# Performance work log

Measured on AMD Instinct MI355X. Metric: run time of the kernel, lower is better.

Reference implementation:

```python
import jax, jax.numpy as jnp
import numpy as np

DMODEL, DK, HEADS, FF = 512, 64, 8, 2048
HD = HEADS * DK  # 512; heads are NOT split in this module
EPS = 1e-5


def layernorm(x, g, b):
    mu = jnp.mean(x, axis=-1, keepdims=True)
    var = jnp.mean(jnp.square(x - mu), axis=-1, keepdims=True)
    return (x - mu) * jax.lax.rsqrt(var + EPS) * g + b


def setup_inputs() -> dict:
    key = jax.random.key(0)
    ks = jax.random.split(key, 20)
    s = 1.0 / np.sqrt(DMODEL)
    u = lambda k, shape, fan: jax.random.uniform(k, shape, jnp.float32, -1.0 / np.sqrt(fan), 1.0 / np.sqrt(fan))
    return {
        "x": jax.random.normal(ks[0], (4, 4096, DMODEL), jnp.float32),
        "Wq_w": u(ks[1], (DMODEL, HD), DMODEL), "Wq_b": u(ks[2], (HD,), DMODEL),
        "Wk_w": u(ks[3], (DMODEL, HD), DMODEL), "Wk_b": u(ks[4], (HD,), DMODEL),
        "Wv_w": u(ks[5], (DMODEL, HD), DMODEL), "Wv_b": u(ks[6], (HD,), DMODEL),
        "Wu_w": u(ks[7], (HD, DMODEL), HD), "Wu_b": u(ks[8], (DMODEL,), HD),
        "ln1_g": jnp.ones((DMODEL,), jnp.float32), "ln1_b": jnp.zeros((DMODEL,), jnp.float32),
        "ff1_w": u(ks[9], (DMODEL, FF), DMODEL), "ff1_b": u(ks[10], (FF,), DMODEL),
        "ff2_w": u(ks[11], (FF, DMODEL), FF), "ff2_b": u(ks[12], (DMODEL,), FF),
        "ln2_g": jnp.ones((DMODEL,), jnp.float32), "ln2_b": jnp.zeros((DMODEL,), jnp.float32),
    }


def reference(x, Wq_w, Wq_b, Wk_w, Wk_b, Wv_w, Wv_b, Wu_w, Wu_b,
              ln1_g, ln1_b, ff1_w, ff1_b, ff2_w, ff2_b, ln2_g, ln2_b):
    # x: (b, n, dmodel). Single encoder layer, faithful to num_encoders=1.
    q = x @ Wq_w + Wq_b            # (b, n, HD)
    k = x @ Wk_w + Wk_b
    v = x @ Wv_w + Wv_b
    # NOTE: original does bmm over full HD dim (no head split), scaled by sqrt(dk)
    scores = jnp.einsum('bnd,bmd->bnm', q, k) / np.sqrt(DK)
    probs = jax.nn.softmax(scores, axis=-1)   # (b, n, n) — O(n^2) materialized as in source
    attn = jnp.einsum('bnm,bmd->bnd', probs, v)
    unified = attn @ Wu_w + Wu_b
    h = layernorm(x + unified, ln1_g, ln1_b)
    ffwd = jax.nn.relu(h @ ff1_w + ff1_b) @ ff2_w + ff2_b
    return layernorm(h + ffwd, ln2_g, ln2_b)
```

## Files before the change

kernel.cpp:

```cpp
#include <hip/hip_runtime.h>

#define AS1 __attribute__((address_space(1)))
#define AS3 __attribute__((address_space(3)))

typedef __attribute__((ext_vector_type(8))) short short8;
typedef __attribute__((ext_vector_type(4))) float floatx4;

__device__ __forceinline__ float b2f(ushort u) {
  union { unsigned int i; float f; } x; x.i = ((unsigned int)u) << 16; return x.f;
}
__device__ __forceinline__ ushort f2b(float f) {
  union { float f; unsigned int i; } x; x.f = f;
  unsigned int r = (x.i + 0x7fffu + ((x.i >> 16) & 1u)) >> 16;
  return (ushort)r;
}

#define GF_RELU 1


__global__ __launch_bounds__(256) void gemm_vw(
    const ushort* __restrict__ qkv, const ushort* __restrict__ wut,
    ushort* __restrict__ vwt)
{
  __shared__ __align__(16) ushort As[128 * 32];
  __shared__ __align__(16) ushort Bs[128 * 32];

  const int id = blockIdx.x;
  const int b  = id >> 7;
  const int t  = id & 127;
  const int bx = t & 31;
  const int by = t >> 5;

  const ushort* A  = wut;
  const ushort* Bt = qkv + (size_t)b * 4096 * 1536 + 1024;
  ushort* C = vwt + (size_t)b * 512 * 4096;

  const int tid  = threadIdx.x;
  const int w    = tid >> 6;
  const int lane = tid & 63;
  const int lo   = lane & 15;
  const int quad = lane >> 4;
  const int m0   = by * 128;
  const int n0   = bx * 128;
  const int wm   = (w & 1) * 64;
  const int wn   = (w >> 1) * 64;

  const int i0 = tid, i1 = tid + 256;
  const ushort* ga0 = A  + (size_t)(m0 + (i0 >> 2)) * 512 + ((i0 & 3) << 3);
  const ushort* ga1 = A  + (size_t)(m0 + (i1 >> 2)) * 512 + ((i1 & 3) << 3);
  const ushort* gb0 = Bt + (size_t)(n0 + (i0 >> 2)) * 1536 + ((i0 & 3) << 3);
  const ushort* gb1 = Bt + (size_t)(n0 + (i1 >> 2)) * 1536 + ((i1 & 3) << 3);

  floatx4 acc[4][4] = {};

  for (int k0 = 0; k0 < 512; k0 += 32) {
    __syncthreads();
    __builtin_amdgcn_global_load_lds((const AS1 void*)(ga0 + k0), (AS3 void*)(As + i0 * 8), 16, 0, 0);
    __builtin_amdgcn_global_load_lds((const AS1 void*)(ga1 + k0), (AS3 void*)(As + i1 * 8), 16, 0, 0);
    __builtin_amdgcn_global_load_lds((const AS1 void*)(gb0 + k0), (AS3 void*)(Bs + i0 * 8), 16, 0, 0);
    __builtin_amdgcn_global_load_lds((const AS1 void*)(gb1 + k0), (AS3 void*)(Bs + i1 * 8), 16, 0, 0);
    __syncthreads();

    short8 af[4], bf[4];
#pragma unroll
    for (int tt = 0; tt < 4; ++tt) {
      af[tt] = *(const short8*)(As + (wm + tt * 16 + lo) * 32 + quad * 8);
      bf[tt] = *(const short8*)(Bs + (wn + tt * 16 + lo) * 32 + quad * 8);
    }
#pragma unroll
    for (int mt = 0; mt < 4; ++mt)
#pragma unroll
      for (int nt = 0; nt < 4; ++nt)
        acc[mt][nt] = __builtin_amdgcn_mfma_f32_16x16x32_bf16(af[mt], bf[nt], acc[mt][nt], 0, 0, 0);
  }

#pragma unroll
  for (int mt = 0; mt < 4; ++mt)
#pragma unroll
    for (int nt = 0; nt < 4; ++nt)
#pragma unroll
      for (int r = 0; r < 4; ++r) {
        const int row = m0 + wm + mt * 16 + quad * 4 + r;
        const int col = n0 + wn + nt * 16 + lo;
        C[(size_t)row * 4096 + col] = f2b(acc[mt][nt][r]);
      }
}

__global__ __launch_bounds__(256) void gemm_qk_exp(
    const ushort* __restrict__ qkv, ushort* __restrict__ P)
{
  __shared__ __align__(16) ushort As[128 * 64];
  __shared__ __align__(16) ushort Bs[128 * 64];

  const int id = blockIdx.x;
  const int b  = id >> 10;
  const int t  = id & 1023;
  const int r8 = t & 7;
  const int s2 = t >> 3;
  const int bx = s2 & 31;
  const int by = r8 + ((s2 >> 5) << 3);

  const ushort* A  = qkv + (size_t)b * 4096 * 1536;
  const ushort* Bt = qkv + (size_t)b * 4096 * 1536 + 512;
  ushort* C = P + (size_t)b * 4096 * 4096;

  const int tid  = threadIdx.x;
  const int w    = tid >> 6;
  const int lane = tid & 63;
  const int lo   = lane & 15;
  const int quad = lane >> 4;
  const int m0   = by * 128;
  const int n0   = bx * 128;
  const int wm   = (w & 1) * 64;
  const int wn   = (w >> 1) * 64;

  const ushort* gaP[4]; const ushort* gbP[4];
#pragma unroll
  for (int k = 0; k < 4; ++k) {
    const int s_ = tid + k * 256;
    const int row = s_ >> 3, sl = s_ & 7;
    gaP[k] = A  + (size_t)(m0 + row) * 1536 + ((sl ^ (row & 7)) << 3);
    gbP[k] = Bt + (size_t)(n0 + row) * 1536 + ((sl ^ (row & 7)) << 3);
  }

  floatx4 acc[4][4] = {};

  for (int k0 = 0; k0 < 512; k0 += 64) {
    __syncthreads();
#pragma unroll
    for (int k = 0; k < 4; ++k) {
      const int s_ = tid + k * 256;
      __builtin_amdgcn_global_load_lds((const AS1 void*)(gaP[k] + k0), (AS3 void*)(As + s_ * 8), 16, 0, 0);
      __builtin_amdgcn_global_load_lds((const AS1 void*)(gbP[k] + k0), (AS3 void*)(Bs + s_ * 8), 16, 0, 0);
    }
    __syncthreads();

#pragma unroll
    for (int kk = 0; kk < 2; ++kk) {
      short8 af[4], bf[4];
#pragma unroll
      for (int tt = 0; tt < 4; ++tt) {
        const int ra = wm + tt * 16 + lo;
        const int rb = wn + tt * 16 + lo;
        af[tt] = *(const short8*)(As + (size_t)ra * 64 + (((kk * 4 + quad) ^ (ra & 7)) << 3));
        bf[tt] = *(const short8*)(Bs + (size_t)rb * 64 + (((kk * 4 + quad) ^ (rb & 7)) << 3));
      }
#pragma unroll
      for (int mt = 0; mt < 4; ++mt)
#pragma unroll
        for (int nt = 0; nt < 4; ++nt)
          acc[mt][nt] = __builtin_amdgcn_mfma_f32_16x16x32_bf16(af[mt], bf[nt], acc[mt][nt], 0, 0, 0);
    }
  }

#pragma unroll
  for (int mt = 0; mt < 4; ++mt)
#pragma unroll
    for (int r = 0; r < 4; ++r) {
      const int row = m0 + wm + mt * 16 + quad * 4 + r;
#pragma unroll
      for (int nt = 0; nt < 4; ++nt) {
        const int col = n0 + wn + nt * 16 + lo;
        C[(size_t)row * 4096 + col] = f2b(__expf(acc[mt][nt][r] * 0.125f));
      }
    }
}

__global__ __launch_bounds__(256) void gemm_pv_wu(
    const ushort* __restrict__ P, const ushort* __restrict__ vwt,
    const float* __restrict__ bias, ushort* __restrict__ uni)
{
  __shared__ __align__(16) ushort As[128 * 64];
  __shared__ __align__(16) ushort Bs[128 * 64];
  __shared__ float rsm[128];

  const int id  = blockIdx.x;
  const int xcd = id & 7;
  const int s   = id >> 3;
  const int bx  = s & 3;
  const int panel = xcd * 16 + (s >> 2);
  const int b  = panel >> 5;
  const int by = panel & 31;

  const ushort* A  = P   + (size_t)b * 4096 * 4096;
  const ushort* Bt = vwt + (size_t)b * 512 * 4096;

  const int tid  = threadIdx.x;
  const int w    = tid >> 6;
  const int lane = tid & 63;
  const int lo   = lane & 15;
  const int quad = lane >> 4;
  const int m0   = by * 128;
  const int n0   = bx * 128;
  const int wm   = (w & 1) * 64;
  const int wn   = (w >> 1) * 64;

  const ushort* gaP[4]; const ushort* gbP[4];
#pragma unroll
  for (int k = 0; k < 4; ++k) {
    const int s_ = tid + k * 256;
    const int row = s_ >> 3, sl = s_ & 7;
    gaP[k] = A  + (size_t)(m0 + row) * 4096 + ((sl ^ (row & 7)) << 3);
    gbP[k] = Bt + (size_t)(n0 + row) * 4096 + ((sl ^ (row & 7)) << 3);
  }

  short8 ones;
#pragma unroll
  for (int j = 0; j < 8; ++j) ones[j] = (short)0x3F80;

  floatx4 acc[4][4] = {};
  floatx4 rsacc[4] = {};

  for (int k0 = 0; k0 < 4096; k0 += 64) {
    __syncthreads();
#pragma unroll
    for (int k = 0; k < 4; ++k) {
      const int s_ = tid + k * 256;
      __builtin_amdgcn_global_load_lds((const AS1 void*)(gaP[k] + k0), (AS3 void*)(As + s_ * 8), 16, 0, 0);
      __builtin_amdgcn_global_load_lds((const AS1 void*)(gbP[k] + k0), (AS3 void*)(Bs + s_ * 8), 16, 0, 0);
    }
    __syncthreads();

#pragma unroll
    for (int kk = 0; kk < 2; ++kk) {
      short8 af[4], bf[4];
#pragma unroll
      for (int tt = 0; tt < 4; ++tt) {
        const int ra = wm + tt * 16 + lo;
        const int rb = wn + tt * 16 + lo;
        af[tt] = *(const short8*)(As + (size_t)ra * 64 + (((kk * 4 + quad) ^ (ra & 7)) << 3));
        bf[tt] = *(const short8*)(Bs + (size_t)rb * 64 + (((kk * 4 + quad) ^ (rb & 7)) << 3));
      }
#pragma unroll
      for (int tt = 0; tt < 4; ++tt)
        rsacc[tt] = __builtin_amdgcn_mfma_f32_16x16x32_bf16(af[tt], ones, rsacc[tt], 0, 0, 0);
#pragma unroll
      for (int mt = 0; mt < 4; ++mt)
#pragma unroll
        for (int nt = 0; nt < 4; ++nt)
          acc[mt][nt] = __builtin_amdgcn_mfma_f32_16x16x32_bf16(af[mt], bf[nt], acc[mt][nt], 0, 0, 0);
    }
  }

  if (wn == 0 && lo == 0) {
#pragma unroll
    for (int tt = 0; tt < 4; ++tt)
#pragma unroll
      for (int r = 0; r < 4; ++r)
        rsm[wm + tt * 16 + quad * 4 + r] = rsacc[tt][r];
  }
  __syncthreads();

#pragma unroll
  for (int mt = 0; mt < 4; ++mt)
#pragma unroll
    for (int r = 0; r < 4; ++r) {
      const int lrow = wm + mt * 16 + quad * 4 + r;
      const size_t grow = (size_t)b * 4096 + m0 + lrow;
      const float inv = 1.f / rsm[lrow];
#pragma unroll
      for (int nt = 0; nt < 4; ++nt) {
        const int col = n0 + wn + nt * 16 + lo;
        uni[grow * 512 + col] = f2b(acc[mt][nt][r] * inv + bias[col]);
      }
    }
}

__global__ __launch_bounds__(256) void gemm_async64(
    const ushort* __restrict__ A, const ushort* __restrict__ Bt,
    const float* __restrict__ bias, ushort* __restrict__ C,
    int N, int K, int lda, int ldb,
    int lg_gx, int lg_gy, float scale, int flags)
{
  __shared__ __align__(16) ushort As[128 * 64];
  __shared__ __align__(16) ushort Bs[128 * 64];

  const int id = blockIdx.x;
  const int r8 = id & 7;
  const int s  = id >> 3;
  const int bx = s & ((1 << lg_gx) - 1);
  const int j  = r8 + ((s >> lg_gx) << 3);
  const int by = j & ((1 << lg_gy) - 1);

  const int tid  = threadIdx.x;
  const int w    = tid >> 6;
  const int lane = tid & 63;
  const int lo   = lane & 15;
  const int quad = lane >> 4;
  const int m0   = by * 128;
  const int n0   = bx * 128;
  const int wm   = (w & 1) * 64;
  const int wn   = (w >> 1) * 64;

  const ushort* gaP[4]; const ushort* gbP[4];
#pragma unroll
  for (int k = 0; k < 4; ++k) {
    const int s_ = tid + k * 256;
    const int row = s_ >> 3, sl = s_ & 7;
    gaP[k] = A  + (size_t)(m0 + row) * lda + ((sl ^ (row & 7)) << 3);
    gbP[k] = Bt + (size_t)(n0 + row) * ldb + ((sl ^ (row & 7)) << 3);
  }

  floatx4 acc[4][4] = {};

  for (int k0 = 0; k0 < K; k0 += 64) {
    __syncthreads();
#pragma unroll
    for (int k = 0; k < 4; ++k) {
      const int s_ = tid + k * 256;
      __builtin_amdgcn_global_load_lds((const AS1 void*)(gaP[k] + k0), (AS3 void*)(As + s_ * 8), 16, 0, 0);
      __builtin_amdgcn_global_load_lds((const AS1 void*)(gbP[k] + k0), (AS3 void*)(Bs + s_ * 8), 16, 0, 0);
    }
    __syncthreads();

#pragma unroll
    for (int kk = 0; kk < 2; ++kk) {
      short8 af[4], bf[4];
#pragma unroll
      for (int tt = 0; tt < 4; ++tt) {
        const int ra = wm + tt * 16 + lo;
        const int rb = wn + tt * 16 + lo;
        af[tt] = *(const short8*)(As + (size_t)ra * 64 + (((kk * 4 + quad) ^ (ra & 7)) << 3));
        bf[tt] = *(const short8*)(Bs + (size_t)rb * 64 + (((kk * 4 + quad) ^ (rb & 7)) << 3));
      }
#pragma unroll
      for (int mt = 0; mt < 4; ++mt)
#pragma unroll
        for (int nt = 0; nt < 4; ++nt)
          acc[mt][nt] = __builtin_amdgcn_mfma_f32_16x16x32_bf16(af[mt], bf[nt], acc[mt][nt], 0, 0, 0);
    }
  }

#pragma unroll
  for (int mt = 0; mt < 4; ++mt)
#pragma unroll
    for (int nt = 0; nt < 4; ++nt)
#pragma unroll
      for (int r = 0; r < 4; ++r) {
        int row = m0 + wm + mt * 16 + quad * 4 + r;
        int col = n0 + wn + nt * 16 + lo;
        float v = acc[mt][nt][r] * scale;
        if (bias) v += bias[col];
        if (flags & GF_RELU) v = fmaxf(v, 0.f);
        C[(size_t)row * N + col] = f2b(v);
      }
}

__global__ __launch_bounds__(256) void gemm_sync_f32a(
    const float* __restrict__ Af, const ushort* __restrict__ Bt,
    const float* __restrict__ bias, ushort* __restrict__ C,
    int N, int K)
{
  __shared__ __align__(16) ushort As[128 * 32];
  __shared__ __align__(16) ushort Bs[128 * 32];

  const int tid  = threadIdx.x;
  const int w    = tid >> 6;
  const int lane = tid & 63;
  const int lo   = lane & 15;
  const int quad = lane >> 4;
  const int m0   = blockIdx.y * 128;
  const int n0   = blockIdx.x * 128;
  const int wm   = (w & 1) * 64;
  const int wn   = (w >> 1) * 64;

  const int i0 = tid, i1 = tid + 256;
  const size_t aoff0 = (size_t)(m0 + (i0 >> 2)) * K + ((i0 & 3) << 3);
  const size_t aoff1 = (size_t)(m0 + (i1 >> 2)) * K + ((i1 & 3) << 3);
  const size_t boff0 = (size_t)(n0 + (i0 >> 2)) * K + ((i0 & 3) << 3);
  const size_t boff1 = (size_t)(n0 + (i1 >> 2)) * K + ((i1 & 3) << 3);

  floatx4 acc[4][4] = {};

  for (int k0 = 0; k0 < K; k0 += 32) {
    short8 va0, va1;
    const float4 a00 = *(const float4*)(Af + aoff0 + k0);
    const float4 a01 = *(const float4*)(Af + aoff0 + k0 + 4);
    const float4 a10 = *(const float4*)(Af + aoff1 + k0);
    const float4 a11 = *(const float4*)(Af + aoff1 + k0 + 4);
    va0[0] = (short)f2b(a00.x); va0[1] = (short)f2b(a00.y);
    va0[2] = (short)f2b(a00.z); va0[3] = (short)f2b(a00.w);
    va0[4] = (short)f2b(a01.x); va0[5] = (short)f2b(a01.y);
    va0[6] = (short)f2b(a01.z); va0[7] = (short)f2b(a01.w);
    va1[0] = (short)f2b(a10.x); va1[1] = (short)f2b(a10.y);
    va1[2] = (short)f2b(a10.z); va1[3] = (short)f2b(a10.w);
    va1[4] = (short)f2b(a11.x); va1[5] = (short)f2b(a11.y);
    va1[6] = (short)f2b(a11.z); va1[7] = (short)f2b(a11.w);
    const short8 vb0 = *(const short8*)(Bt + boff0 + k0);
    const short8 vb1 = *(const short8*)(Bt + boff1 + k0);
    __syncthreads();
    *(short8*)(As + i0 * 8) = va0;
    *(short8*)(As + i1 * 8) = va1;
    *(short8*)(Bs + i0 * 8) = vb0;
    *(short8*)(Bs + i1 * 8) = vb1;
    __syncthreads();

    short8 af[4], bf[4];
#pragma unroll
    for (int t = 0; t < 4; ++t) {
      af[t] = *(const short8*)(As + (wm + t * 16 + lo) * 32 + quad * 8);
      bf[t] = *(const short8*)(Bs + (wn + t * 16 + lo) * 32 + quad * 8);
    }
#pragma unroll
    for (int mt = 0; mt < 4; ++mt)
#pragma unroll
      for (int nt = 0; nt < 4; ++nt)
        acc[mt][nt] = __builtin_amdgcn_mfma_f32_16x16x32_bf16(af[mt], bf[nt], acc[mt][nt], 0, 0, 0);
  }

#pragma unroll
  for (int mt = 0; mt < 4; ++mt)
#pragma unroll
    for (int nt = 0; nt < 4; ++nt)
#pragma unroll
      for (int r = 0; r < 4; ++r) {
        int row = m0 + wm + mt * 16 + quad * 4 + r;
        int col = n0 + wn + nt * 16 + lo;
        C[(size_t)row * N + col] = f2b(acc[mt][nt][r] + bias[col]);
      }
}

__global__ void transpose_cast(const float* __restrict__ in, ushort* __restrict__ out,
                               int R, int C)
{
  __shared__ ushort t[64][65];
  const int r0 = blockIdx.y * 64, c0 = blockIdx.x * 64;
  const int tx = threadIdx.x, ty = threadIdx.y;
  for (int i = ty; i < 64; i += 4)
    t[i][tx] = f2b(in[(size_t)(r0 + i) * C + c0 + tx]);
  __syncthreads();
  for (int i = ty; i < 64; i += 4)
    out[(size_t)(c0 + i) * R + r0 + tx] = t[tx][i];
}

__global__ void concat_bias(const float* __restrict__ a, const float* __restrict__ b,
                            const float* __restrict__ c, float* __restrict__ o)
{
  const int i = blockIdx.x * 256 + threadIdx.x;
  o[i] = (i < 512) ? a[i] : ((i < 1024) ? b[i - 512] : c[i - 1024]);
}

__global__ __launch_bounds__(256) void ln_res(
    const void* __restrict__ Xv, int x_f32, const ushort* __restrict__ Y,
    const float* __restrict__ g, const float* __restrict__ b,
    void* __restrict__ outv, int o_f32)
{
  const int w = threadIdx.x >> 6, lane = threadIdx.x & 63;
  const size_t row = (size_t)blockIdx.x * 4 + w;
  const size_t base = row * 512 + lane * 8;

  float v[8];
  if (x_f32) {
    const float* X = (const float*)Xv + base;
    const float4 x0 = *(const float4*)(X), x1 = *(const float4*)(X + 4);
    v[0] = x0.x; v[1] = x0.y; v[2] = x0.z; v[3] = x0.w;
    v[4] = x1.x; v[5] = x1.y; v[6] = x1.z; v[7] = x1.w;
  } else {
    const short8 xv = *(const short8*)((const ushort*)Xv + base);
#pragma unroll
    for (int j = 0; j < 8; ++j) v[j] = b2f((ushort)xv[j]);
  }
  const short8 yv = *(const short8*)(Y + base);
  float s = 0.f, sq = 0.f;
#pragma unroll
  for (int j = 0; j < 8; ++j) {
    v[j] += b2f((ushort)yv[j]);
    s += v[j]; sq += v[j] * v[j];
  }
  for (int m = 1; m < 64; m <<= 1) {
    s  += __shfl_xor(s,  m, 64);
    sq += __shfl_xor(sq, m, 64);
  }
  const float mean = s * (1.f / 512.f);
  const float var  = sq * (1.f / 512.f) - mean * mean;
  const float rstd = rsqrtf(fmaxf(var, 0.f) + 1e-5f);

  const float4 g0 = *(const float4*)(g + lane * 8);
  const float4 g1 = *(const float4*)(g + lane * 8 + 4);
  const float4 b0 = *(const float4*)(b + lane * 8);
  const float4 b1 = *(const float4*)(b + lane * 8 + 4);
  const float gg[8] = {g0.x, g0.y, g0.z, g0.w, g1.x, g1.y, g1.z, g1.w};
  const float bb[8] = {b0.x, b0.y, b0.z, b0.w, b1.x, b1.y, b1.z, b1.w};

  if (o_f32) {
    float* o = (float*)outv + base;
#pragma unroll
    for (int j = 0; j < 8; ++j) o[j] = (v[j] - mean) * rstd * gg[j] + bb[j];
  } else {
    ushort* o = (ushort*)outv + base;
    short8 ov;
#pragma unroll
    for (int j = 0; j < 8; ++j) ov[j] = (short)f2b((v[j] - mean) * rstd * gg[j] + bb[j]);
    *(short8*)o = ov;
  }
}

extern "C" void kernel_launch(void* const* d_in, const int* in_sizes, int n_in,
                              void* d_out, int out_size, void* d_ws, size_t ws_size,
                              hipStream_t stream)
{
  const float* x    = (const float*)d_in[0];
  const float* Wq_w = (const float*)d_in[1];
  const float* Wq_b = (const float*)d_in[2];
  const float* Wk_w = (const float*)d_in[3];
  const float* Wk_b = (const float*)d_in[4];
  const float* Wv_w = (const float*)d_in[5];
  const float* Wv_b = (const float*)d_in[6];
  const float* Wu_w = (const float*)d_in[7];
  const float* Wu_b = (const float*)d_in[8];
  const float* g1   = (const float*)d_in[9];
  const float* b1   = (const float*)d_in[10];
  const float* f1w  = (const float*)d_in[11];
  const float* f1b  = (const float*)d_in[12];
  const float* f2w  = (const float*)d_in[13];
  const float* f2bv = (const float*)d_in[14];
  const float* g2   = (const float*)d_in[15];
  const float* b2   = (const float*)d_in[16];

  char* wsb = (char*)d_ws;
  ushort* wqkvt = (ushort*)(wsb + 0);
  ushort* wut   = (ushort*)(wsb + 1572864);
  ushort* f1t   = (ushort*)(wsb + 2097152);
  ushort* f2t   = (ushort*)(wsb + 4194304);
  float*  bqkv  = (float*) (wsb + 6291456);
  ushort* qkv   = (ushort*)(wsb + 6297600);
  ushort* vwt   = (ushort*)(wsb + 56629248);
  ushort* uni   = (ushort*)(wsb + 73406464);
  ushort* h     = (ushort*)(wsb + 106960896);
  ushort* mid   = (ushort*)(wsb + 123738112);
  ushort* ffo   = (ushort*)(wsb + 190846976);
  ushort* Pbuf  = (ushort*)(wsb + 90183680);

  const dim3 tb(64, 4);
  transpose_cast<<<dim3(8, 8),  tb, 0, stream>>>(Wq_w, wqkvt,              512, 512);
  transpose_cast<<<dim3(8, 8),  tb, 0, stream>>>(Wk_w, wqkvt + 512 * 512,  512, 512);
  transpose_cast<<<dim3(8, 8),  tb, 0, stream>>>(Wv_w, wqkvt + 1024 * 512, 512, 512);
  transpose_cast<<<dim3(8, 8),  tb, 0, stream>>>(Wu_w, wut, 512, 512);
  transpose_cast<<<dim3(32, 8), tb, 0, stream>>>(f1w, f1t, 512, 2048);
  transpose_cast<<<dim3(8, 32), tb, 0, stream>>>(f2w, f2t, 2048, 512);
  concat_bias<<<6, 256, 0, stream>>>(Wq_b, Wk_b, Wv_b, bqkv);

  gemm_sync_f32a<<<dim3(12, 128), 256, 0, stream>>>(x, wqkvt, bqkv, qkv, 1536, 512);

  gemm_vw<<<512, 256, 0, stream>>>(qkv, wut, vwt);
  gemm_qk_exp<<<4096, 256, 0, stream>>>(qkv, Pbuf);
  gemm_pv_wu<<<512, 256, 0, stream>>>(Pbuf, vwt, Wu_b, uni);

  ln_res<<<4096, 256, 0, stream>>>(x, 1, uni, g1, b1, h, 0);

  gemm_async64<<<2048, 256, 0, stream>>>(h, f1t, f1b, mid,
      2048, 512, 512, 512, 4, 7, 1.f, GF_RELU);
  gemm_async64<<<512, 256, 0, stream>>>(mid, f2t, f2bv, ffo,
      512, 2048, 2048, 2048, 2, 7, 1.f, 0);
  ln_res<<<4096, 256, 0, stream>>>(h, 0, ffo, g2, b2, d_out, 1);
}
```

Measured before the change: 512.1 us.

## Stage GEMM epilogues through LDS for coalesced stores, remap QK grid, async QKV GEMM

The QK-exp and async GEMM epilogues now write results into a swizzled shared-memory tile and then emit 16-byte coalesced global stores, replacing scattered 2-byte stores. The QK-exp block index mapping is changed to group blocks by XCD per batch and row panel. The QKV projection now casts x to bf16 in a separate pass and uses a 64-wide K loop with global_load_lds in place of the synchronous fp32-input GEMM. This costs an extra cast kernel, extra traffic for the bf16 copy of x, and extra barriers in each epilogue.

```diff
diff --git a/kernel.cpp b/kernel.cpp
--- a/kernel.cpp
+++ b/kernel.cpp
@@ -89,16 +89,16 @@
 __global__ __launch_bounds__(256) void gemm_qk_exp(
     const ushort* __restrict__ qkv, ushort* __restrict__ P)
 {
-  __shared__ __align__(16) ushort As[128 * 64];
-  __shared__ __align__(16) ushort Bs[128 * 64];
-
-  const int id = blockIdx.x;
-  const int b  = id >> 10;
-  const int t  = id & 1023;
-  const int r8 = t & 7;
-  const int s2 = t >> 3;
-  const int bx = s2 & 31;
-  const int by = r8 + ((s2 >> 5) << 3);
+  __shared__ __align__(16) ushort smem[128 * 128];
+  ushort* As = smem;
+  ushort* Bs = smem + 128 * 64;
+
+  const int id  = blockIdx.x;
+  const int xcd = id & 7;
+  const int s   = id >> 3;
+  const int b   = xcd >> 1;
+  const int by  = (xcd & 1) * 16 + (s & 15);
+  const int bx  = s >> 4;
 
   const ushort* A  = qkv + (size_t)b * 4096 * 1536;
   const ushort* Bt = qkv + (size_t)b * 4096 * 1536 + 512;
@@ -153,17 +153,27 @@
     }
   }
 
+  __syncthreads();
 #pragma unroll
   for (int mt = 0; mt < 4; ++mt)
 #pragma unroll
     for (int r = 0; r < 4; ++r) {
-      const int row = m0 + wm + mt * 16 + quad * 4 + r;
+      const int row = wm + mt * 16 + quad * 4 + r;
 #pragma unroll
       for (int nt = 0; nt < 4; ++nt) {
-        const int col = n0 + wn + nt * 16 + lo;
-        C[(size_t)row * 4096 + col] = f2b(__expf(acc[mt][nt][r] * 0.125f));
-      }
-    }
+        const int col = wn + nt * 16 + lo;
+        smem[row * 128 + ((((col >> 3) ^ (row & 7)) << 3) | (col & 7))] =
+            f2b(__expf(acc[mt][nt][r] * 0.125f));
+      }
+    }
+  __syncthreads();
+#pragma unroll
+  for (int k = 0; k < 8; ++k) {
+    const int c = tid + k * 256;
+    const int row = c >> 4, c16 = c & 15;
+    const short8 v = *(const short8*)(smem + row * 128 + ((c16 ^ (row & 7)) << 3));
+    *(short8*)(C + (size_t)(m0 + row) * 4096 + n0 + c16 * 8) = v;
+  }
 }
 
 __global__ __launch_bounds__(256) void gemm_pv_wu(
@@ -272,8 +282,9 @@
     int N, int K, int lda, int ldb,
     int lg_gx, int lg_gy, float scale, int flags)
 {
-  __shared__ __align__(16) ushort As[128 * 64];
-  __shared__ __align__(16) ushort Bs[128 * 64];
+  __shared__ __align__(16) ushort smem[128 * 128];
+  ushort* As = smem;
+  ushort* Bs = smem + 128 * 64;
 
   const int id = blockIdx.x;
   const int r8 = id & 7;
@@ -331,93 +342,126 @@
     }
   }
 
+  __syncthreads();
 #pragma unroll
   for (int mt = 0; mt < 4; ++mt)
 #pragma unroll
-    for (int nt = 0; nt < 4; ++nt)
-#pragma unroll
-      for (int r = 0; r < 4; ++r) {
-        int row = m0 + wm + mt * 16 + quad * 4 + r;
-        int col = n0 + wn + nt * 16 + lo;
+    for (int r = 0; r < 4; ++r) {
+      const int row = wm + mt * 16 + quad * 4 + r;
+#pragma unroll
+      for (int nt = 0; nt < 4; ++nt) {
+        const int col = wn + nt * 16 + lo;
         float v = acc[mt][nt][r] * scale;
-        if (bias) v += bias[col];
+        if (bias) v += bias[n0 + col];
         if (flags & GF_RELU) v = fmaxf(v, 0.f);
-        C[(size_t)row * N + col] = f2b(v);
-      }
-}
-
-__global__ __launch_bounds__(256) void gemm_sync_f32a(
-    const float* __restrict__ Af, const ushort* __restrict__ Bt,
-    const float* __restrict__ bias, ushort* __restrict__ C,
-    int N, int K)
-{
-  __shared__ __align__(16) ushort As[128 * 32];
-  __shared__ __align__(16) ushort Bs[128 * 32];
+        smem[row * 128 + ((((col >> 3) ^ (row & 7)) << 3) | (col & 7))] = f2b(v);
+      }
+    }
+  __syncthreads();
+#pragma unroll
+  for (int k = 0; k < 8; ++k) {
+    const int c = tid + k * 256;
+    const int row = c >> 4, c16 = c & 15;
+    const short8 v = *(const short8*)(smem + row * 128 + ((c16 ^ (row & 7)) << 3));
+    *(short8*)(C + (size_t)(m0 + row) * N + n0 + c16 * 8) = v;
+  }
+}
+
+__global__ __launch_bounds__(256) void gemm_qkv(
+    const ushort* __restrict__ A, const ushort* __restrict__ Bt,
+    const float* __restrict__ bias, ushort* __restrict__ C)
+{
+  __shared__ __align__(16) ushort smem[128 * 128];
+  ushort* As = smem;
+  ushort* Bs = smem + 128 * 64;
+
+  const int bx = blockIdx.x;
+  const int by = blockIdx.y;
 
   const int tid  = threadIdx.x;
   const int w    = tid >> 6;
   const int lane = tid & 63;
   const int lo   = lane & 15;
   const int quad = lane >> 4;
-  const int m0   = blockIdx.y * 128;
-  const int n0   = blockIdx.x * 128;
+  const int m0   = by * 128;
+  const int n0   = bx * 128;
   const int wm   = (w & 1) * 64;
   const int wn   = (w >> 1) * 64;
 
-  const int i0 = tid, i1 = tid + 256;
-  const size_t aoff0 = (size_t)(m0 + (i0 >> 2)) * K + ((i0 & 3) << 3);
-  const size_t aoff1 = (size_t)(m0 + (i1 >> 2)) * K + ((i1 & 3) << 3);
-  const size_t boff0 = (size_t)(n0 + (i0 >> 2)) * K + ((i0 & 3) << 3);
-  const size_t boff1 = (size_t)(n0 + (i1 >> 2)) * K + ((i1 & 3) << 3);
+  const ushort* gaP[4]; const ushort* gbP[4];
+#pragma unroll
+  for (int k = 0; k < 4; ++k) {
+    const int s_ = tid + k * 256;
+    const int row = s_ >> 3, sl = s_ & 7;
+    gaP[k] = A  + (size_t)(m0 + row) * 512 + ((sl ^ (row & 7)) << 3);
+    gbP[k] = Bt + (size_t)(n0 + row) * 512 + ((sl ^ (row & 7)) << 3);
+  }
 
   floatx4 acc[4][4] = {};
 
-  for (int k0 = 0; k0 < K; k0 += 32) {
-    short8 va0, va1;
-    const float4 a00 = *(const float4*)(Af + aoff0 + k0);
-    const float4 a01 = *(const float4*)(Af + aoff0 + k0 + 4);
-    const float4 a10 = *(const float4*)(Af + aoff1 + k0);
-    const float4 a11 = *(const float4*)(Af + aoff1 + k0 + 4);
-    va0[0] = (short)f2b(a00.x); va0[1] = (short)f2b(a00.y);
-    va0[2] = (short)f2b(a00.z); va0[3] = (short)f2b(a00.w);
-    va0[4] = (short)f2b(a01.x); va0[5] = (short)f2b(a01.y);
-    va0[6] = (short)f2b(a01.z); va0[7] = (short)f2b(a01.w);
-    va1[0] = (short)f2b(a10.x); va1[1] = (short)f2b(a10.y);
-    va1[2] = (short)f2b(a10.z); va1[3] = (short)f2b(a10.w);
-    va1[4] = (short)f2b(a11.x); va1[5] = (short)f2b(a11.y);
-    va1[6] = (short)f2b(a11.z); va1[7] = (short)f2b(a11.w);
-    const short8 vb0 = *(const short8*)(Bt + boff0 + k0);
-    const short8 vb1 = *(const short8*)(Bt + boff1 + k0);
-    __syncthreads();
-    *(short8*)(As + i0 * 8) = va0;
-    *(short8*)(As + i1 * 8) = va1;
-    *(short8*)(Bs + i0 * 8) = vb0;
-    *(short8*)(Bs + i1 * 8) = vb1;
-    __syncthreads();
-
-    short8 af[4], bf[4];
-#pragma unroll
-    for (int t = 0; t < 4; ++t) {
-      af[t] = *(const short8*)(As + (wm + t * 16 + lo) * 32 + quad * 8);
-      bf[t] = *(const short8*)(Bs + (wn + t * 16 + lo) * 32 + quad * 8);
-    }
-#pragma unroll
-    for (int mt = 0; mt < 4; ++mt)
-#pragma unroll
-      for (int nt = 0; nt < 4; ++nt)
-        acc[mt][nt] = __builtin_amdgcn_mfma_f32_16x16x32_bf16(af[mt], bf[nt], acc[mt][nt], 0, 0, 0);
-  }
-
+  for (int k0 = 0; k0 < 512; k0 += 64) {
+    __syncthreads();
+#pragma unroll
+    for (int k = 0; k < 4; ++k) {
+      const int s_ = tid + k * 256;
+      __builtin_amdgcn_global_load_lds((const AS1 void*)(gaP[k] + k0), (AS3 void*)(As + s_ * 8), 16, 0, 0);
+      __builtin_amdgcn_global_load_lds((const AS1 void*)(gbP[k] + k0), (AS3 void*)(Bs + s_ * 8), 16, 0, 0);
+    }
+    __syncthreads();
+
+#pragma unroll
+    for (int kk = 0; kk < 2; ++kk) {
+      short8 af[4], bf[4];
+#pragma unroll
+      for (int tt = 0; tt < 4; ++tt) {
+        const int ra = wm + tt * 16 + lo;
+        const int rb = wn + tt * 16 + lo;
+        af[tt] = *(const short8*)(As + (size_t)ra * 64 + (((kk * 4 + quad) ^ (ra & 7)) << 3));
+        bf[tt] = *(const short8*)(Bs + (size_t)rb * 64 + (((kk * 4 + quad) ^ (rb & 7)) << 3));
+      }
+#pragma unroll
+      for (int mt = 0; mt < 4; ++mt)
+#pragma unroll
+        for (int nt = 0; nt < 4; ++nt)
+          acc[mt][nt] = __builtin_amdgcn_mfma_f32_16x16x32_bf16(af[mt], bf[nt], acc[mt][nt], 0, 0, 0);
+    }
+  }
+
+  __syncthreads();
 #pragma unroll
   for (int mt = 0; mt < 4; ++mt)
 #pragma unroll
-    for (int nt = 0; nt < 4; ++nt)
-#pragma unroll
-      for (int r = 0; r < 4; ++r) {
-        int row = m0 + wm + mt * 16 + quad * 4 + r;
-        int col = n0 + wn + nt * 16 + lo;
-        C[(size_t)row * N + col] = f2b(acc[mt][nt][r] + bias[col]);
-      }
+    for (int r = 0; r < 4; ++r) {
+      const int row = wm + mt * 16 + quad * 4 + r;
+#pragma unroll
+      for (int nt = 0; nt < 4; ++nt) {
+        const int col = wn + nt * 16 + lo;
+        smem[row * 128 + ((((col >> 3) ^ (row & 7)) << 3) | (col & 7))] =
+            f2b(acc[mt][nt][r] + bias[n0 + col]);
+      }
+    }
+  __syncthreads();
+#pragma unroll
+  for (int k = 0; k < 8; ++k) {
+    const int c = tid + k * 256;
+    const int row = c >> 4, c16 = c & 15;
+    const short8 v = *(const short8*)(smem + row * 128 + ((c16 ^ (row & 7)) << 3));
+    *(short8*)(C + (size_t)(m0 + row) * 1536 + n0 + c16 * 8) = v;
+  }
+}
+
+__global__ __launch_bounds__(256) void cast_f32_bf16(
+    const float* __restrict__ in, ushort* __restrict__ out)
+{
+  const size_t i = ((size_t)blockIdx.x * 256 + threadIdx.x) * 8;
+  const float4 a = *(const float4*)(in + i);
+  const float4 b = *(const float4*)(in + i + 4);
+  short8 v;
+  v[0] = (short)f2b(a.x); v[1] = (short)f2b(a.y);
+  v[2] = (short)f2b(a.z); v[3] = (short)f2b(a.w);
+  v[4] = (short)f2b(b.x); v[5] = (short)f2b(b.y);
+  v[6] = (short)f2b(b.z); v[7] = (short)f2b(b.w);
+  *(short8*)(out + i) = v;
 }
 
 __global__ void transpose_cast(const float* __restrict__ in, ushort* __restrict__ out,
@@ -530,6 +574,7 @@
   ushort* mid   = (ushort*)(wsb + 123738112);
   ushort* ffo   = (ushort*)(wsb + 190846976);
   ushort* Pbuf  = (ushort*)(wsb + 90183680);
+  ushort* xb    = (ushort*)(wsb + 90183680);
 
   const dim3 tb(64, 4);
   transpose_cast<<<dim3(8, 8),  tb, 0, stream>>>(Wq_w, wqkvt,              512, 512);
@@ -540,7 +585,8 @@
   transpose_cast<<<dim3(8, 32), tb, 0, stream>>>(f2w, f2t, 2048, 512);
   concat_bias<<<6, 256, 0, stream>>>(Wq_b, Wk_b, Wv_b, bqkv);
 
-  gemm_sync_f32a<<<dim3(12, 128), 256, 0, stream>>>(x, wqkvt, bqkv, qkv, 1536, 512);
+  cast_f32_bf16<<<4096, 256, 0, stream>>>(x, xb);
+  gemm_qkv<<<dim3(12, 128), 256, 0, stream>>>(xb, wqkvt, bqkv, qkv);
 
   gemm_vw<<<512, 256, 0, stream>>>(qkv, wut, vwt);
   gemm_qk_exp<<<4096, 256, 0, stream>>>(qkv, Pbuf);
```

New measurement: 512.0 us. Within noise of the previous version (-0.0%).
